# Performance work log

Hardware: AMD Instinct MI355X
Metric: run time of the kernel (lower is better)

## Reference

```python
import jax, jax.numpy as jnp
import numpy as np

B, N, C, H, L, D_FF = 32, 196, 768, 12, 4, 3072

def _ln(x, g, b, eps=1e-6):
    m = x.mean(-1, keepdims=True)
    v = ((x - m) ** 2).mean(-1, keepdims=True)
    return (x - m) / jnp.sqrt(v + eps) * g + b

def _sdpa(q, k, v, scale):
    a = jax.nn.softmax(jnp.einsum('...qd,...kd->...qk', q, k) * scale, axis=-1)
    return jnp.einsum('...qk,...kd->...qd', a, v)

def _vit_attn(x, qkv_w, qkv_b, proj_w, proj_b):
    Bs, Ns, Cs = x.shape
    hd = Cs // H
    qkv = (x @ qkv_w + qkv_b).reshape(Bs, Ns, 3, H, hd).transpose(2, 0, 3, 1, 4)
    q, k, v = qkv[0], qkv[1], qkv[2]  # [B,H,N,hd]
    o = _sdpa(q, k, v, hd ** -0.5).transpose(0, 2, 1, 3).reshape(Bs, Ns, Cs)
    return o @ proj_w + proj_b

def _mlp(x, w1, b1, w2, b2):
    return jax.nn.gelu(x @ w1 + b1, approximate=False) @ w2 + b2

def setup_inputs() -> dict:
    key = jax.random.key(0)
    ks = jax.random.split(key, 16)
    w = lambda k, s: (jax.random.normal(k, s, jnp.float32) * 0.02)
    inp = {
        'x': jax.random.normal(ks[0], (B, N, C), jnp.float32),
        'y': jax.random.normal(ks[1], (B, N, C), jnp.float32),
        'latents': w(ks[2], (1, L, C)),
        'scale_a': jnp.zeros((1,), jnp.float32),
        'scale_v': jnp.zeros((1,), jnp.float32),
    }
    for i, p in enumerate(['s', 'r']):
        kk = jax.random.split(ks[3 + i], 4)
        inp.update({
            f'{p}_ln1_g': jnp.ones((C,), jnp.float32),
            f'{p}_ln1_b': jnp.zeros((C,), jnp.float32),
            f'{p}_qkv_w': w(kk[0], (C, 3 * C)),
            f'{p}_qkv_b': jnp.zeros((3 * C,), jnp.float32),
            f'{p}_proj_w': w(kk[1], (C, C)),
            f'{p}_proj_b': jnp.zeros((C,), jnp.float32),
            f'{p}_ln2_g': jnp.ones((C,), jnp.float32),
            f'{p}_ln2_b': jnp.zeros((C,), jnp.float32),
            f'{p}_fc1_w': w(kk[2], (C, D_FF)),
            f'{p}_fc1_b': jnp.zeros((D_FF,), jnp.float32),
            f'{p}_fc2_w': w(kk[3], (D_FF, C)),
            f'{p}_fc2_b': jnp.zeros((C,), jnp.float32),
        })
    return inp

def reference(x, y, latents, scale_a, scale_v,
              s_ln1_g, s_ln1_b, s_qkv_w, s_qkv_b, s_proj_w, s_proj_b,
              s_ln2_g, s_ln2_b, s_fc1_w, s_fc1_b, s_fc2_w, s_fc2_b,
              r_ln1_g, r_ln1_b, r_qkv_w, r_qkv_b, r_proj_w, r_proj_b,
              r_ln2_g, r_ln2_b, r_fc1_w, r_fc1_b, r_fc2_w, r_fc2_b):
    BS = x.shape[0]
    Cf = x.shape[-1]
    # --- latent bottleneck fusion (single-head, scale = C**-0.5) ---
    concat = jnp.concatenate([x, y], axis=1)            # [B, Na+Nv, C]
    lat = jnp.broadcast_to(latents, (BS,) + latents.shape[1:])
    fused = _sdpa(lat, concat, concat, Cf ** -0.5)      # [B, L, C]
    x = x + scale_a * _sdpa(x, fused, fused, Cf ** -0.5)
    y = y + scale_v * _sdpa(y, fused, fused, Cf ** -0.5)
    # --- standard ViT blocks per stream ---
    x = x + _vit_attn(_ln(x, s_ln1_g, s_ln1_b), s_qkv_w, s_qkv_b, s_proj_w, s_proj_b)
    y = y + _vit_attn(_ln(y, r_ln1_g, r_ln1_b), r_qkv_w, r_qkv_b, r_proj_w, r_proj_b)
    x = x + _mlp(_ln(x, s_ln2_g, s_ln2_b), s_fc1_w, s_fc1_b, s_fc2_w, s_fc2_b)
    y = y + _mlp(_ln(y, r_ln2_g, r_ln2_b), r_fc1_w, r_fc1_b, r_fc2_w, r_fc2_b)
    return (x, y)
```

## Files before the change

### kernel.cpp

```cpp
#include <hip/hip_runtime.h>
#include <hip/hip_bf16.h>
#include <math.h>

constexpr int Bc   = 32;
constexpr int Nc   = 196;
constexpr int Cc   = 768;
constexpr int Hc   = 12;
constexpr int HDc  = 64;
constexpr int Lc   = 4;
constexpr int DFFc = 3072;
constexpr int NCAT = 2 * Nc;
constexpr int Mrows = Bc * Nc;
constexpr float SCALE_C = 0.03608439182435161f;
constexpr float SCALE_H = 0.125f;
constexpr float LOG2E   = 1.4426950408889634f;

typedef __attribute__((ext_vector_type(8))) short short8;
typedef __attribute__((ext_vector_type(4))) short s16x4;
typedef __attribute__((ext_vector_type(4))) float float4a;
typedef __attribute__((ext_vector_type(4))) _Float16 half4;

__device__ inline float gelu_fast(float v) {
    float c = v * (0.7978845608028654f + 0.035677408136300125f * v * v);
    float ex = __expf(2.f * c);
    float th = 1.f - 2.f / (ex + 1.f);
    return 0.5f * v * (1.f + th);
}

__device__ inline void store_val(float* p, float v) { *p = v; }
__device__ inline void store_val(__hip_bfloat16* p, float v) { *p = __float2bfloat16(v); }

__device__ inline void gload16(const void* g, void* l) {
    __builtin_amdgcn_global_load_lds(
        (const __attribute__((address_space(1))) void*)g,
        (__attribute__((address_space(3))) void*)l, 16, 0, 0);
}

__global__ __launch_bounds__(256) void lat_scores_ker(
    const float* __restrict__ x, const float* __restrict__ y,
    const float* __restrict__ lat, float* __restrict__ scores)
{
    int wglobal = blockIdx.x * 4 + (threadIdx.x >> 6);
    int lane = threadIdx.x & 63;
    int b = wglobal / NCAT, j = wglobal % NCAT;
    const float* row = (j < Nc) ? x + ((size_t)b * Nc + j) * Cc
                                : y + ((size_t)b * Nc + (j - Nc)) * Cc;
    float a0 = 0.f, a1 = 0.f, a2 = 0.f, a3 = 0.f;
    for (int c = lane; c < Cc; c += 64) {
        float rv = row[c];
        a0 += rv * lat[c];
        a1 += rv * lat[Cc + c];
        a2 += rv * lat[2 * Cc + c];
        a3 += rv * lat[3 * Cc + c];
    }
    #pragma unroll
    for (int o = 32; o; o >>= 1) {
        a0 += __shfl_xor(a0, o);
        a1 += __shfl_xor(a1, o);
        a2 += __shfl_xor(a2, o);
        a3 += __shfl_xor(a3, o);
    }
    if (lane == 0) {
        float* sb = scores + (size_t)b * Lc * NCAT + j;
        sb[0 * NCAT] = a0 * SCALE_C;
        sb[1 * NCAT] = a1 * SCALE_C;
        sb[2 * NCAT] = a2 * SCALE_C;
        sb[3 * NCAT] = a3 * SCALE_C;
    }
}

__global__ __launch_bounds__(256) void lat_softmax_ker(float* __restrict__ scores)
{
    int b = blockIdx.x;
    int w = threadIdx.x >> 6, lane = threadIdx.x & 63;
    float* row = scores + (size_t)b * Lc * NCAT + w * NCAT;
    float m = -INFINITY;
    for (int j = lane; j < NCAT; j += 64) m = fmaxf(m, row[j]);
    #pragma unroll
    for (int o = 32; o; o >>= 1) m = fmaxf(m, __shfl_xor(m, o));
    float sum = 0.f;
    float e0 = expf(row[lane] - m);
    float e1 = expf(row[lane + 64] - m);
    float e2 = expf(row[lane + 128] - m);
    float e3 = expf(row[lane + 192] - m);
    float e4 = expf(row[lane + 256] - m);
    float e5 = expf(row[lane + 320] - m);
    float e6 = (lane < 8) ? expf(row[lane + 384] - m) : 0.f;
    sum = e0 + e1 + e2 + e3 + e4 + e5 + e6;
    #pragma unroll
    for (int o = 32; o; o >>= 1) sum += __shfl_xor(sum, o);
    float inv = 1.f / sum;
    row[lane] = e0 * inv;
    row[lane + 64] = e1 * inv;
    row[lane + 128] = e2 * inv;
    row[lane + 192] = e3 * inv;
    row[lane + 256] = e4 * inv;
    row[lane + 320] = e5 * inv;
    if (lane < 8) row[lane + 384] = e6 * inv;
}

__global__ __launch_bounds__(256) void lat_fused_ker(
    const float* __restrict__ x, const float* __restrict__ y,
    const float* __restrict__ probs, float* __restrict__ fused)
{
    int b = blockIdx.x, chunk = blockIdx.y;
    int t = threadIdx.x;
    int l = t >> 6;
    int c = chunk * 64 + (t & 63);
    __shared__ float p[Lc][NCAT];
    for (int idx = t; idx < Lc * NCAT; idx += 256)
        (&p[0][0])[idx] = probs[(size_t)b * Lc * NCAT + idx];
    __syncthreads();

    float acc0 = 0.f, acc1 = 0.f;
    for (int j = 0; j < Nc; j += 2) {
        const float* r0 = x + ((size_t)b * Nc + j) * Cc;
        acc0 += p[l][j] * r0[c];
        acc1 += p[l][j + 1] * r0[Cc + c];
    }
    for (int j = 0; j < Nc; j += 2) {
        const float* r0 = y + ((size_t)b * Nc + j) * Cc;
        acc0 += p[l][Nc + j] * r0[c];
        acc1 += p[l][Nc + j + 1] * r0[Cc + c];
    }
    fused[(size_t)b * Lc * Cc + l * Cc + c] = acc0 + acc1;
}

__global__ __launch_bounds__(256) void inject_ker(
    const float* __restrict__ x, const float* __restrict__ y,
    const float* __restrict__ fused,
    const float* __restrict__ scale_a, const float* __restrict__ scale_v,
    float* __restrict__ out)
{
    int gid = blockIdx.x;
    int st = gid / Mrows;
    int bn = gid % Mrows;
    int b = bn / Nc;
    const float* src = st ? y : x;
    float scale = st ? scale_v[0] : scale_a[0];
    float* dst = out + (size_t)st * Mrows * Cc;
    const float* f = fused + (size_t)b * Lc * Cc;
    const float* row = src + (size_t)bn * Cc;

    __shared__ float sc[4];
    int w = threadIdx.x >> 6, lane = threadIdx.x & 63;
    float partial = 0.f;
    for (int c = lane; c < Cc; c += 64) partial += row[c] * f[w * Cc + c];
    #pragma unroll
    for (int o = 32; o; o >>= 1) partial += __shfl_xor(partial, o);
    if (lane == 0) sc[w] = partial * SCALE_C;
    __syncthreads();

    float s0 = sc[0], s1 = sc[1], s2 = sc[2], s3 = sc[3];
    float m = fmaxf(fmaxf(s0, s1), fmaxf(s2, s3));
    float e0 = expf(s0 - m), e1 = expf(s1 - m), e2 = expf(s2 - m), e3 = expf(s3 - m);
    float inv = 1.f / (e0 + e1 + e2 + e3);
    e0 *= inv; e1 *= inv; e2 *= inv; e3 *= inv;

    for (int c = threadIdx.x; c < Cc; c += 256) {
        float v = e0 * f[c] + e1 * f[Cc + c] + e2 * f[2 * Cc + c] + e3 * f[3 * Cc + c];
        dst[(size_t)bn * Cc + c] = row[c] + scale * v;
    }
}

__global__ __launch_bounds__(256) void inject_ln_ker(
    const float* __restrict__ x, const float* __restrict__ y,
    const float* __restrict__ fusedb,
    const float* __restrict__ scale_a, const float* __restrict__ scale_v,
    const float* __restrict__ ga, const float* __restrict__ ba,
    const float* __restrict__ gv, const float* __restrict__ bv,
    float* __restrict__ out, __hip_bfloat16* __restrict__ lnout, size_t lnz)
{
    int gid = blockIdx.x;
    int st = gid / Mrows;
    int bn = gid % Mrows;
    int b = bn / Nc;
    const float* src = st ? y : x;
    float scale = st ? scale_v[0] : scale_a[0];
    const float* g  = st ? gv : ga;
    const float* bb = st ? bv : ba;
    float* dst = out + (size_t)st * Mrows * Cc + (size_t)bn * Cc;
    __hip_bfloat16* lno = lnout + (size_t)st * lnz + (size_t)bn * Cc;
    const float* f = fusedb + (size_t)b * Lc * Cc;
    const float* row = src + (size_t)bn * Cc;

    __shared__ float sc[4];
    __shared__ float red[4];
    int t = threadIdx.x;
    int w = t >> 6, lane = t & 63;
    float partial = 0.f;
    for (int c = lane; c < Cc; c += 64) partial += row[c] * f[w * Cc + c];
    #pragma unroll
    for (int o = 32; o; o >>= 1) partial += __shfl_xor(partial, o);
    if (lane == 0) sc[w] = partial * SCALE_C;
    __syncthreads();

    float s0 = sc[0], s1 = sc[1], s2 = sc[2], s3 = sc[3];
    float m = fmaxf(fmaxf(s0, s1), fmaxf(s2, s3));
    float e0 = expf(s0 - m), e1 = expf(s1 - m), e2 = expf(s2 - m), e3 = expf(s3 - m);
    float inv = 1.f / (e0 + e1 + e2 + e3);
    e0 *= inv; e1 *= inv; e2 *= inv; e3 *= inv;

    float u[3];
    float s = 0.f;
    #pragma unroll
    for (int k = 0; k < 3; ++k) {
        int c = t + 256 * k;
        float v = e0 * f[c] + e1 * f[Cc + c] + e2 * f[2 * Cc + c] + e3 * f[3 * Cc + c];
        u[k] = row[c] + scale * v;
        s += u[k];
    }
    #pragma unroll
    for (int o = 32; o; o >>= 1) s += __shfl_xor(s, o);
    if (lane == 0) red[w] = s;
    __syncthreads();
    float mean = (red[0] + red[1] + red[2] + red[3]) * (1.f / Cc);

    float vs = 0.f;
    #pragma unroll
    for (int k = 0; k < 3; ++k) { float d = u[k] - mean; vs += d * d; }
    #pragma unroll
    for (int o = 32; o; o >>= 1) vs += __shfl_xor(vs, o);
    __syncthreads();
    if (lane == 0) red[w] = vs;
    __syncthreads();
    float var = (red[0] + red[1] + red[2] + red[3]) * (1.f / Cc);
    float rinv = 1.f / sqrtf(var + 1e-6f);

    #pragma unroll
    for (int k = 0; k < 3; ++k) {
        int c = t + 256 * k;
        dst[c] = u[k];
        lno[c] = __float2bfloat16((u[k] - mean) * rinv * g[c] + bb[c]);
    }
}

__global__ __launch_bounds__(256) void ln_ker(
    const float* __restrict__ in, size_t inz,
    const float* __restrict__ g0, const float* __restrict__ b0,
    const float* __restrict__ g1, const float* __restrict__ b1,
    __hip_bfloat16* __restrict__ out, size_t outz)
{
    int z = blockIdx.z;
    const float* g = z ? g1 : g0;
    const float* bb = z ? b1 : b0;
    in += (size_t)z * inz; out += (size_t)z * outz;

    int row = blockIdx.x;
    __shared__ float buf[Cc];
    __shared__ float red[4];
    __shared__ float red2[4];
    const float* r = in + (size_t)row * Cc;
    int w = threadIdx.x >> 6, lane = threadIdx.x & 63;

    float s = 0.f;
    for (int c = threadIdx.x; c < Cc; c += 256) {
        float v = r[c];
        buf[c] = v;
        s += v;
    }
    #pragma unroll
    for (int o = 32; o; o >>= 1) s += __shfl_xor(s, o);
    if (lane == 0) red[w] = s;
    __syncthreads();
    float mean = (red[0] + red[1] + red[2] + red[3]) * (1.f / Cc);

    float vs = 0.f;
    for (int c = threadIdx.x; c < Cc; c += 256) {
        float d = buf[c] - mean;
        vs += d * d;
    }
    #pragma unroll
    for (int o = 32; o; o >>= 1) vs += __shfl_xor(vs, o);
    if (lane == 0) red2[w] = vs;
    __syncthreads();
    float var = (red2[0] + red2[1] + red2[2] + red2[3]) * (1.f / Cc);
    float inv = 1.f / sqrtf(var + 1e-6f);

    for (int c = threadIdx.x; c < Cc; c += 256)
        out[(size_t)row * Cc + c] =
            __float2bfloat16((buf[c] - mean) * inv * g[c] + bb[c]);
}

struct WArgs {
    const float* src[8];
    __hip_bfloat16* dst[8];
};

__global__ __launch_bounds__(256) void wcast_all_ker(WArgs wa)
{
    int z = blockIdx.z;
    int bx = blockIdx.x;
    int which, tile, K_, N_;
    if (bx < 1728)      { which = 0; tile = bx;        K_ = 768;  N_ = 2304; }
    else if (bx < 2304) { which = 1; tile = bx - 1728; K_ = 768;  N_ = 768;  }
    else if (bx < 4608) { which = 2; tile = bx - 2304; K_ = 768;  N_ = 3072; }
    else                { which = 3; tile = bx - 4608; K_ = 3072; N_ = 768;  }
    const float* W = wa.src[z * 4 + which];
    __hip_bfloat16* WT = wa.dst[z * 4 + which];
    int ntx = N_ >> 5;
    int n0 = (tile % ntx) * 32, k0 = (tile / ntx) * 32;

    __shared__ float tilebuf[32][33];
    int t = threadIdx.x;
    int r = t >> 5, c = t & 31;
    #pragma unroll
    for (int p = 0; p < 4; ++p)
        tilebuf[r + p * 8][c] = W[(size_t)(k0 + r + p * 8) * N_ + n0 + c];
    __syncthreads();
    #pragma unroll
    for (int p = 0; p < 4; ++p)
        WT[(size_t)(n0 + r + p * 8) * K_ + k0 + c] =
            __float2bfloat16(tilebuf[c][r + p * 8]);
}

template <int EPI, typename OutT>
__global__ __launch_bounds__(256, 2) void gemm_bf16_ker(
    const __hip_bfloat16* __restrict__ A, size_t Az,
    const __hip_bfloat16* __restrict__ BT, size_t BTz,
    const float* __restrict__ bias0, const float* __restrict__ bias1,
    const float* __restrict__ res, size_t resz,
    OutT* __restrict__ out, size_t outz,
    int M_, int N_, int K_)
{
    const int gx = gridDim.x, gy = gridDim.y;
    const long T = (long)gx * gy * gridDim.z;
    long iflat = blockIdx.x + (long)gx * (blockIdx.y + (long)gy * blockIdx.z);
    long q = T >> 3, r = T & 7;
    long xcd = iflat & 7, jj = iflat >> 3;
    long tt = (xcd < r ? xcd * (q + 1) : r * (q + 1) + (xcd - r) * q) + jj;
    const int bx = (int)(tt % gx);
    const int by = (int)((tt / gx) % gy);
    const int z  = (int)(tt / ((long)gx * gy));

    A += (size_t)z * Az;
    BT += (size_t)z * BTz;
    const float* bias = z ? bias1 : bias0;
    res += (size_t)z * resz;
    out += (size_t)z * outz;

    __shared__ short As[128 * 32];
    __shared__ short Bs[128 * 32];
    const int t = threadIdx.x;
    const int wid = t >> 6, lane = t & 63;
    const int row0 = by * 128, col0 = bx * 128;
    const int wr = (wid >> 1) * 64, wc = (wid & 1) * 64;

    const int f0 = wid * 1024 + lane * 16;
    const int f1 = f0 + 4096;
    const int r0s = f0 >> 6, r1s = f1 >> 6;
    const int u0 = ((f0 >> 4) & 3) ^ ((r0s >> 1) & 3);
    const int u1 = ((f1 >> 4) & 3) ^ ((r1s >> 1) & 3);

    const __hip_bfloat16* aS0 = A + (size_t)(row0 + r0s) * K_ + u0 * 8;
    const __hip_bfloat16* aS1 = A + (size_t)(row0 + r1s) * K_ + u1 * 8;
    const __hip_bfloat16* bS0 = BT + (size_t)(col0 + r0s) * K_ + u0 * 8;
    const __hip_bfloat16* bS1 = BT + (size_t)(col0 + r1s) * K_ + u1 * 8;
    short* ldsA0 = As + (wid * 1024) / 2;
    short* ldsA1 = As + (4096 + wid * 1024) / 2;
    short* ldsB0 = Bs + (wid * 1024) / 2;
    short* ldsB1 = Bs + (4096 + wid * 1024) / 2;

    const int fr = lane & 15;
    const int ku = lane >> 4;

    float4a acc[4][4];
    #pragma unroll
    for (int m = 0; m < 4; ++m)
        #pragma unroll
        for (int n = 0; n < 4; ++n)
            acc[m][n] = (float4a)0.f;

    for (int kt = 0; kt < K_; kt += 32) {
        gload16(aS0 + kt, ldsA0);
        gload16(aS1 + kt, ldsA1);
        gload16(bS0 + kt, ldsB0);
        gload16(bS1 + kt, ldsB1);
        __syncthreads();

        short8 af[4], bf8[4];
        #pragma unroll
        for (int m = 0; m < 4; ++m) {
            int rl = wr + m * 16 + fr;
            int swz = ku ^ ((rl >> 1) & 3);
            af[m] = *(const short8*)(As + rl * 32 + swz * 8);
        }
        #pragma unroll
        for (int n = 0; n < 4; ++n) {
            int cl = wc + n * 16 + fr;
            int swz = ku ^ ((cl >> 1) & 3);
            bf8[n] = *(const short8*)(Bs + cl * 32 + swz * 8);
        }
        #pragma unroll
        for (int m = 0; m < 4; ++m)
            #pragma unroll
            for (int n = 0; n < 4; ++n)
                acc[m][n] = __builtin_amdgcn_mfma_f32_16x16x32_bf16(
                    af[m], bf8[n], acc[m][n], 0, 0, 0);
        __syncthreads();
    }

    const int fq = lane >> 4;
    #pragma unroll
    for (int m = 0; m < 4; ++m) {
        #pragma unroll
        for (int n = 0; n < 4; ++n) {
            int col = col0 + wc + n * 16 + fr;
            float b = bias[col];
            #pragma unroll
            for (int j = 0; j < 4; ++j) {
                int row = row0 + wr + m * 16 + fq * 4 + j;
                float v = acc[m][n][j] + b;
                if (EPI == 1) v = gelu_fast(v);
                if (EPI == 2) v += res[(size_t)row * N_ + col];
                store_val(out + (size_t)row * N_ + col, v);
            }
        }
    }
}

constexpr int NKT = 13;
constexpr int NQT = 13;
constexpr int NPAD = NKT * 16;
constexpr int VTS = 216;

__global__ __launch_bounds__(256) void attn_mfma_ker(
    const __hip_bfloat16* __restrict__ qkv, size_t qz,
    __hip_bfloat16* __restrict__ o, size_t oz)
{
    int z = blockIdx.z;
    qkv += (size_t)z * qz;
    o += (size_t)z * oz;

    int h = blockIdx.x, b = blockIdx.y;
    __shared__ short Ks[NPAD * 64];
    __shared__ _Float16 VT[64 * VTS];
    const size_t rs = 3 * Cc;
    const __hip_bfloat16* base = qkv + (size_t)b * Nc * rs + h * HDc;
    const int t = threadIdx.x;

    for (int c = t; c < NPAD * 8; c += 256) {
        int row = c >> 3, u = c & 7;
        int srow = row < Nc ? row : Nc - 1;
        short8 kv = *(const short8*)(base + (size_t)srow * rs + Cc + u * 8);
        *(short8*)(Ks + row * 64 + ((u ^ (row & 7)) << 3)) = kv;
        short8 vv = *(const short8*)(base + (size_t)srow * rs + 2 * Cc + u * 8);
        #pragma unroll
        for (int w = 0; w < 8; ++w) {
            __hip_bfloat16 bvv = ((const __hip_bfloat16*)&vv)[w];
            VT[(u * 8 + w) * VTS + row] = (_Float16)__bfloat162float(bvv);
        }
    }
    __syncthreads();

    const int wv = t >> 6, lane = t & 63;
    const int g = lane >> 4, c16 = lane & 15;
    const float KS = SCALE_H * LOG2E;

    for (int qt = wv; qt < NQT; qt += 4) {
        int qrow = qt * 16 + c16;
        int sq = qrow < Nc ? qrow : Nc - 1;
        const __hip_bfloat16* qb = base + (size_t)sq * rs + g * 8;
        short8 bq0 = *(const short8*)(qb);
        short8 bq1 = *(const short8*)(qb + 32);

        float4a acc[NKT];
        #pragma unroll
        for (int kt = 0; kt < NKT; ++kt) acc[kt] = (float4a)0.f;
        #pragma unroll
        for (int kt = 0; kt < NKT; ++kt) {
            int r = kt * 16 + c16;
            short8 a0 = *(const short8*)(Ks + r * 64 + ((g ^ (r & 7)) << 3));
            short8 a1 = *(const short8*)(Ks + r * 64 + (((4 + g) ^ (r & 7)) << 3));
            acc[kt] = __builtin_amdgcn_mfma_f32_16x16x32_bf16(a0, bq0, acc[kt], 0, 0, 0);
            acc[kt] = __builtin_amdgcn_mfma_f32_16x16x32_bf16(a1, bq1, acc[kt], 0, 0, 0);
        }

        float m = -INFINITY;
        #pragma unroll
        for (int kt = 0; kt < NKT; ++kt) {
            #pragma unroll
            for (int j = 0; j < 4; ++j) {
                int key = kt * 16 + g * 4 + j;
                float v = (key < Nc) ? acc[kt][j] * KS : -INFINITY;
                acc[kt][j] = v;
                m = fmaxf(m, v);
            }
        }
        m = fmaxf(m, __shfl_xor(m, 16));
        m = fmaxf(m, __shfl_xor(m, 32));

        float sum = 0.f;
        half4 pb[NKT];
        #pragma unroll
        for (int kt = 0; kt < NKT; ++kt) {
            #pragma unroll
            for (int j = 0; j < 4; ++j) {
                float e = exp2f(acc[kt][j] - m);
                sum += e;
                pb[kt][j] = (_Float16)e;
            }
        }
        sum += __shfl_xor(sum, 16);
        sum += __shfl_xor(sum, 32);
        float inv = 1.f / sum;

        float4a oa[4];
        #pragma unroll
        for (int dt = 0; dt < 4; ++dt) oa[dt] = (float4a)0.f;
        #pragma unroll
        for (int kt = 0; kt < NKT; ++kt) {
            #pragma unroll
            for (int dt = 0; dt < 4; ++dt) {
                half4 av = *(const half4*)(VT + (size_t)(dt * 16 + c16) * VTS
                                              + kt * 16 + g * 4);
                oa[dt] = __builtin_amdgcn_mfma_f32_16x16x16f16(av, pb[kt], oa[dt], 0, 0, 0);
            }
        }

        if (qrow < Nc) {
            __hip_bfloat16* ob = o + ((size_t)b * Nc + qrow) * Cc + h * HDc;
            #pragma unroll
            for (int dt = 0; dt < 4; ++dt) {
                __hip_bfloat16 tmp[4];
                #pragma unroll
                for (int j = 0; j < 4; ++j)
                    tmp[j] = __float2bfloat16(oa[dt][j] * inv);
                *(s16x4*)(ob + dt * 16 + g * 4) = *(const s16x4*)tmp;
            }
        }
    }
}

extern "C" void kernel_launch(void* const* d_in, const int* in_sizes, int n_in,
                              void* d_out, int out_size, void* d_ws, size_t ws_size,
                              hipStream_t stream)
{
    const float* x       = (const float*)d_in[0];
    const float* y       = (const float*)d_in[1];
    const float* latents = (const float*)d_in[2];
    const float* scale_a = (const float*)d_in[3];
    const float* scale_v = (const float*)d_in[4];

    float* out = (float*)d_out;

    constexpr size_t WSTREAM = 7077888;
    constexpr size_t OFF_QKV = 0;
    constexpr size_t OFF_PROJ = 2304 * 768;
    constexpr size_t OFF_FC1 = OFF_PROJ + 768 * 768;
    constexpr size_t OFF_FC2 = OFF_FC1 + 3072 * 768;

    constexpr size_t FRONT = ((size_t)Bc * Lc * NCAT + (size_t)Bc * Lc * Cc) * 4;
    constexpr size_t NEED_BATCH = FRONT
        + 2 * (size_t)Mrows * Cc * 2
        + 2 * (size_t)Mrows * DFFc * 2
        + 2 * WSTREAM * 2;

    float* ws = (float*)d_ws;
    float* scores = ws;
    float* fusedb = scores + (size_t)Bc * Lc * NCAT;

    const bool batched = ws_size >= NEED_BATCH;

    __hip_bfloat16* tbuf = (__hip_bfloat16*)(fusedb + (size_t)Bc * Lc * Cc);
    __hip_bfloat16* big;
    __hip_bfloat16* wT;
    if (batched) {
        big = tbuf + 2 * (size_t)Mrows * Cc;
        wT  = big + 2 * (size_t)Mrows * DFFc;
    } else {
        big = tbuf + (size_t)Mrows * Cc;
        wT  = big + (size_t)Mrows * DFFc;
    }

    lat_scores_ker<<<Bc * NCAT / 4, 256, 0, stream>>>(x, y, latents, scores);
    lat_softmax_ker<<<Bc, 256, 0, stream>>>(scores);
    lat_fused_ker<<<dim3(Bc, 12), 256, 0, stream>>>(x, y, scores, fusedb);

    WArgs wa;
    for (int p = 0; p < 2; ++p) {
        int basei = 5 + 12 * p;
        wa.src[p * 4 + 0] = (const float*)d_in[basei + 2];
        wa.src[p * 4 + 1] = (const float*)d_in[basei + 4];
        wa.src[p * 4 + 2] = (const float*)d_in[basei + 8];
        wa.src[p * 4 + 3] = (const float*)d_in[basei + 10];
        wa.dst[p * 4 + 0] = wT + p * WSTREAM + OFF_QKV;
        wa.dst[p * 4 + 1] = wT + p * WSTREAM + OFF_PROJ;
        wa.dst[p * 4 + 2] = wT + p * WSTREAM + OFF_FC1;
        wa.dst[p * 4 + 3] = wT + p * WSTREAM + OFF_FC2;
    }

    const float* g1[2], *b1[2], *qkvb[2], *projb[2], *g2[2], *b2[2], *fc1b[2], *fc2b[2];
    for (int p = 0; p < 2; ++p) {
        int basei = 5 + 12 * p;
        g1[p]    = (const float*)d_in[basei + 0];
        b1[p]    = (const float*)d_in[basei + 1];
        qkvb[p]  = (const float*)d_in[basei + 3];
        projb[p] = (const float*)d_in[basei + 5];
        g2[p]    = (const float*)d_in[basei + 6];
        b2[p]    = (const float*)d_in[basei + 7];
        fc1b[p]  = (const float*)d_in[basei + 9];
        fc2b[p]  = (const float*)d_in[basei + 11];
    }

    const size_t MC = (size_t)Mrows * Cc;
    const size_t MQKV = (size_t)Mrows * 2304;
    const size_t MFF = (size_t)Mrows * DFFc;

    if (batched) {
        inject_ln_ker<<<2 * Mrows, 256, 0, stream>>>(
            x, y, fusedb, scale_a, scale_v,
            g1[0], b1[0], g1[1], b1[1], out, tbuf, MC);
        wcast_all_ker<<<dim3(6912, 1, 2), 256, 0, stream>>>(wa);
        gemm_bf16_ker<0, __hip_bfloat16><<<dim3(18, 49, 2), 256, 0, stream>>>(
            tbuf, MC, wT + OFF_QKV, WSTREAM, qkvb[0], qkvb[1],
            (const float*)out, 0, big, MQKV, Mrows, 2304, 768);
        attn_mfma_ker<<<dim3(Hc, Bc, 2), 256, 0, stream>>>(big, MQKV, tbuf, MC);
        gemm_bf16_ker<2, float><<<dim3(6, 49, 2), 256, 0, stream>>>(
            tbuf, MC, wT + OFF_PROJ, WSTREAM, projb[0], projb[1],
            (const float*)out, MC, out, MC, Mrows, 768, 768);
        ln_ker<<<dim3(Mrows, 1, 2), 256, 0, stream>>>(
            out, MC, g2[0], b2[0], g2[1], b2[1], tbuf, MC);
        gemm_bf16_ker<1, __hip_bfloat16><<<dim3(24, 49, 2), 256, 0, stream>>>(
            tbuf, MC, wT + OFF_FC1, WSTREAM, fc1b[0], fc1b[1],
            (const float*)out, 0, big, MFF, Mrows, 3072, 768);
        gemm_bf16_ker<2, float><<<dim3(6, 49, 2), 256, 0, stream>>>(
            big, MFF, wT + OFF_FC2, WSTREAM, fc2b[0], fc2b[1],
            (const float*)out, MC, out, MC, Mrows, 768, 3072);
    } else {
        inject_ker<<<2 * Mrows, 256, 0, stream>>>(x, y, fusedb, scale_a, scale_v, out);
        wcast_all_ker<<<dim3(6912, 1, 2), 256, 0, stream>>>(wa);
        for (int p = 0; p < 2; ++p) {
            float* X = out + (size_t)p * MC;
            __hip_bfloat16* wb = wT + p * WSTREAM;
            ln_ker<<<dim3(Mrows, 1, 1), 256, 0, stream>>>(
                X, 0, g1[p], b1[p], g1[p], b1[p], tbuf, 0);
            gemm_bf16_ker<0, __hip_bfloat16><<<dim3(18, 49, 1), 256, 0, stream>>>(
                tbuf, 0, wb + OFF_QKV, 0, qkvb[p], qkvb[p],
                (const float*)X, 0, big, 0, Mrows, 2304, 768);
            attn_mfma_ker<<<dim3(Hc, Bc, 1), 256, 0, stream>>>(big, 0, tbuf, 0);
            gemm_bf16_ker<2, float><<<dim3(6, 49, 1), 256, 0, stream>>>(
                tbuf, 0, wb + OFF_PROJ, 0, projb[p], projb[p],
                (const float*)X, 0, X, 0, Mrows, 768, 768);
            ln_ker<<<dim3(Mrows, 1, 1), 256, 0, stream>>>(
                X, 0, g2[p], b2[p], g2[p], b2[p], tbuf, 0);
            gemm_bf16_ker<1, __hip_bfloat16><<<dim3(24, 49, 1), 256, 0, stream>>>(
                tbuf, 0, wb + OFF_FC1, 0, fc1b[p], fc1b[p],
                (const float*)X, 0, big, 0, Mrows, 3072, 768);
            gemm_bf16_ker<2, float><<<dim3(6, 49, 1), 256, 0, stream>>>(
                big, 0, wb + OFF_FC2, 0, fc2b[p], fc2b[p],
                (const float*)X, 0, X, 0, Mrows, 768, 3072);
        }
    }
}
```

Baseline: 442.4 us.

## Double-buffer GEMM LDS tiles and fold latent softmax into fused kernel

The bf16 MFMA GEMM now keeps two LDS buffers for A and B and issues the global-to-LDS loads for the next K tile before computing on the current one. This removes one barrier per iteration and lets load latency overlap with MFMA work, at the cost of doubling LDS use per block, which may lower occupancy. Separately, the latent softmax kernel is removed and its work is done inside lat_fused_ker on the shared-memory copy of the scores, saving a launch and a global round trip. Each of the 12 chunk blocks now recomputes that softmax redundantly.

Measured after the change: 444.8 us, median of 2. No clear change (+0.6%).

```diff
diff --git a/kernel.cpp b/kernel.cpp
--- a/kernel.cpp
+++ b/kernel.cpp
@@ -69,49 +69,37 @@
     }
 }
 
-__global__ __launch_bounds__(256) void lat_softmax_ker(float* __restrict__ scores)
-{
-    int b = blockIdx.x;
-    int w = threadIdx.x >> 6, lane = threadIdx.x & 63;
-    float* row = scores + (size_t)b * Lc * NCAT + w * NCAT;
-    float m = -INFINITY;
-    for (int j = lane; j < NCAT; j += 64) m = fmaxf(m, row[j]);
-    #pragma unroll
-    for (int o = 32; o; o >>= 1) m = fmaxf(m, __shfl_xor(m, o));
-    float sum = 0.f;
-    float e0 = expf(row[lane] - m);
-    float e1 = expf(row[lane + 64] - m);
-    float e2 = expf(row[lane + 128] - m);
-    float e3 = expf(row[lane + 192] - m);
-    float e4 = expf(row[lane + 256] - m);
-    float e5 = expf(row[lane + 320] - m);
-    float e6 = (lane < 8) ? expf(row[lane + 384] - m) : 0.f;
-    sum = e0 + e1 + e2 + e3 + e4 + e5 + e6;
-    #pragma unroll
-    for (int o = 32; o; o >>= 1) sum += __shfl_xor(sum, o);
-    float inv = 1.f / sum;
-    row[lane] = e0 * inv;
-    row[lane + 64] = e1 * inv;
-    row[lane + 128] = e2 * inv;
-    row[lane + 192] = e3 * inv;
-    row[lane + 256] = e4 * inv;
-    row[lane + 320] = e5 * inv;
-    if (lane < 8) row[lane + 384] = e6 * inv;
-}
-
 __global__ __launch_bounds__(256) void lat_fused_ker(
     const float* __restrict__ x, const float* __restrict__ y,
-    const float* __restrict__ probs, float* __restrict__ fused)
+    const float* __restrict__ scores, float* __restrict__ fused)
 {
     int b = blockIdx.x, chunk = blockIdx.y;
     int t = threadIdx.x;
-    int l = t >> 6;
-    int c = chunk * 64 + (t & 63);
     __shared__ float p[Lc][NCAT];
     for (int idx = t; idx < Lc * NCAT; idx += 256)
-        (&p[0][0])[idx] = probs[(size_t)b * Lc * NCAT + idx];
-    __syncthreads();
-
+        (&p[0][0])[idx] = scores[(size_t)b * Lc * NCAT + idx];
+    __syncthreads();
+    int w = t >> 6, lane = t & 63;
+    {
+        float m = -INFINITY;
+        for (int j = lane; j < NCAT; j += 64) m = fmaxf(m, p[w][j]);
+        #pragma unroll
+        for (int o = 32; o; o >>= 1) m = fmaxf(m, __shfl_xor(m, o));
+        float sum = 0.f;
+        for (int j = lane; j < NCAT; j += 64) {
+            float e = expf(p[w][j] - m);
+            p[w][j] = e;
+            sum += e;
+        }
+        #pragma unroll
+        for (int o = 32; o; o >>= 1) sum += __shfl_xor(sum, o);
+        float inv = 1.f / sum;
+        for (int j = lane; j < NCAT; j += 64) p[w][j] *= inv;
+    }
+    __syncthreads();
+
+    int l = w;
+    int c = chunk * 64 + lane;
     float acc0 = 0.f, acc1 = 0.f;
     for (int j = 0; j < Nc; j += 2) {
         const float* r0 = x + ((size_t)b * Nc + j) * Cc;
@@ -339,8 +327,8 @@
     res += (size_t)z * resz;
     out += (size_t)z * outz;
 
-    __shared__ short As[128 * 32];
-    __shared__ short Bs[128 * 32];
+    __shared__ short As[2][128 * 32];
+    __shared__ short Bs[2][128 * 32];
     const int t = threadIdx.x;
     const int wid = t >> 6, lane = t & 63;
     const int row0 = by * 128, col0 = bx * 128;
@@ -356,10 +344,8 @@
     const __hip_bfloat16* aS1 = A + (size_t)(row0 + r1s) * K_ + u1 * 8;
     const __hip_bfloat16* bS0 = BT + (size_t)(col0 + r0s) * K_ + u0 * 8;
     const __hip_bfloat16* bS1 = BT + (size_t)(col0 + r1s) * K_ + u1 * 8;
-    short* ldsA0 = As + (wid * 1024) / 2;
-    short* ldsA1 = As + (4096 + wid * 1024) / 2;
-    short* ldsB0 = Bs + (wid * 1024) / 2;
-    short* ldsB1 = Bs + (4096 + wid * 1024) / 2;
+    const int o0 = (wid * 1024) >> 1;
+    const int o1 = (4096 + wid * 1024) >> 1;
 
     const int fr = lane & 15;
     const int ku = lane >> 4;
@@ -371,25 +357,35 @@
         for (int n = 0; n < 4; ++n)
             acc[m][n] = (float4a)0.f;
 
+#define STAGE(B, KT)                                  \
+    {                                                 \
+        gload16(aS0 + (KT), &As[B][o0]);              \
+        gload16(aS1 + (KT), &As[B][o1]);              \
+        gload16(bS0 + (KT), &Bs[B][o0]);              \
+        gload16(bS1 + (KT), &Bs[B][o1]);              \
+    }
+
+    STAGE(0, 0);
+    __syncthreads();
+
+    int cur = 0;
     for (int kt = 0; kt < K_; kt += 32) {
-        gload16(aS0 + kt, ldsA0);
-        gload16(aS1 + kt, ldsA1);
-        gload16(bS0 + kt, ldsB0);
-        gload16(bS1 + kt, ldsB1);
-        __syncthreads();
-
+        if (kt + 32 < K_) STAGE(cur ^ 1, kt + 32);
+
+        const short* Ab = As[cur];
+        const short* Bb = Bs[cur];
         short8 af[4], bf8[4];
         #pragma unroll
         for (int m = 0; m < 4; ++m) {
             int rl = wr + m * 16 + fr;
             int swz = ku ^ ((rl >> 1) & 3);
-            af[m] = *(const short8*)(As + rl * 32 + swz * 8);
+            af[m] = *(const short8*)(Ab + rl * 32 + swz * 8);
         }
         #pragma unroll
         for (int n = 0; n < 4; ++n) {
             int cl = wc + n * 16 + fr;
             int swz = ku ^ ((cl >> 1) & 3);
-            bf8[n] = *(const short8*)(Bs + cl * 32 + swz * 8);
+            bf8[n] = *(const short8*)(Bb + cl * 32 + swz * 8);
         }
         #pragma unroll
         for (int m = 0; m < 4; ++m)
@@ -397,8 +393,11 @@
             for (int n = 0; n < 4; ++n)
                 acc[m][n] = __builtin_amdgcn_mfma_f32_16x16x32_bf16(
                     af[m], bf8[n], acc[m][n], 0, 0, 0);
+
         __syncthreads();
-    }
+        cur ^= 1;
+    }
+#undef STAGE
 
     const int fq = lane >> 4;
     #pragma unroll
@@ -574,7 +573,6 @@
     }
 
     lat_scores_ker<<<Bc * NCAT / 4, 256, 0, stream>>>(x, y, latents, scores);
-    lat_softmax_ker<<<Bc, 256, 0, stream>>>(scores);
     lat_fused_ker<<<dim3(Bc, 12), 256, 0, stream>>>(x, y, scores, fusedb);
 
     WArgs wa;
```
